# Optimization experiments

Hardware: AMD Instinct MI355X
Metric: run time of the kernel (lower is better)

The kernel has to match this reference:

```python
import jax, jax.numpy as jnp
import numpy as np


def setup_inputs() -> dict:
    key = jax.random.key(0)
    ks = jax.random.split(key, 32)
    B, S, H, E, Vs, T = 32, 400, 512, 300, 200, 32
    EN, V = 50000, 50200
    rn = lambda k, shape, s=0.05: jax.random.normal(k, shape, jnp.float32) * s
    return {
        'encoder_hidden': rn(ks[0], (B, S, 2 * H), 1.0),
        'hidden0': rn(ks[1], (B, H), 1.0),
        'user_embed': rn(ks[2], (B, E), 1.0),
        'W_embed': rn(ks[3], (EN, E), 1.0),
        'W_ih': rn(ks[4], (3 * H, E)), 'W_hh': rn(ks[5], (3 * H, H)),
        'b_ih': rn(ks[6], (3 * H,)), 'b_hh': rn(ks[7], (3 * H,)),
        'Wk_c': rn(ks[8], (2 * H, H)), 'bk_c': rn(ks[9], (H,)),
        'Wq_c': rn(ks[10], (H, H)), 'bq_c': rn(ks[11], (H,)),
        'we_c': rn(ks[12], (H,)), 'be_c': rn(ks[13], (1,)),
        'Wk_u': rn(ks[14], (E, H)), 'bk_u': rn(ks[15], (H,)),
        'Wq_u': rn(ks[16], (H, H)), 'bq_u': rn(ks[17], (H,)),
        'we_u': rn(ks[18], (H,)), 'be_u': rn(ks[19], (1,)),
        'Wc': rn(ks[20], (3 * H + 2 * E, H)),
        'Wg': rn(ks[21], (3 * H + E,)), 'bg': rn(ks[22], (1,)),
        'Wgen': rn(ks[23], (H, EN)),
        'src_mask': jnp.ones((B, S), jnp.int32),
        'tgt_': jax.random.randint(ks[24], (B, T), 0, EN),
        'specific_vocab': jax.random.randint(ks[25], (B, Vs), 0, EN),
        'vocab_size': V,
    }


def reference(encoder_hidden, hidden0, user_embed, W_embed, W_ih, W_hh, b_ih, b_hh,
              Wk_c, bk_c, Wq_c, bq_c, we_c, be_c, Wk_u, bk_u, Wq_u, bq_u, we_u, be_u,
              Wc, Wg, bg, Wgen, src_mask, tgt_, specific_vocab, vocab_size):
    B, T = tgt_.shape
    # teacher forcing: prev token embed, step 0 uses <s> token id 1
    tgt_embed = W_embed[tgt_]                                  # [B,T,E]
    init_embed = jnp.broadcast_to(W_embed[1], (B, 1, W_embed.shape[1]))
    prev = jnp.concatenate([init_embed, tgt_embed[:, :T - 1]], axis=1)
    xs = jnp.swapaxes(prev, 0, 1)                              # [T,B,E]

    user_vocab_emb = W_embed[specific_vocab]                   # [B,Vs,E]
    proj_key_c = encoder_hidden @ Wk_c + bk_c                  # [B,S,H]
    proj_key_u = user_vocab_emb @ Wk_u + bk_u                  # [B,Vs,H]
    mask = src_mask != 0
    batch_idx = jnp.arange(B)[:, None]

    def gru_cell(h, x):
        gi = x @ W_ih.T + b_ih
        gh = h @ W_hh.T + b_hh
        i_r, i_z, i_n = jnp.split(gi, 3, axis=-1)
        h_r, h_z, h_n = jnp.split(gh, 3, axis=-1)
        r = jax.nn.sigmoid(i_r + h_r)
        z = jax.nn.sigmoid(i_z + h_z)
        n = jnp.tanh(i_n + r * h_n)
        return (1.0 - z) * n + z * h

    def step(h, x):
        h = gru_cell(h, x)                                     # [B,H]
        q = h
        # Bahdanau attention over encoder states
        sc = jnp.tanh((q @ Wq_c + bq_c)[:, None, :] + proj_key_c) @ we_c + be_c  # [B,S]
        sc = jnp.where(mask, sc, -1e9)
        ac = jax.nn.softmax(sc, axis=-1)
        ctx_c = jnp.einsum('bs,bsd->bd', ac, encoder_hidden)   # [B,2H]
        # Bahdanau attention over user-specific vocab embeddings
        su = jnp.tanh((q @ Wq_u + bq_u)[:, None, :] + proj_key_u) @ we_u + be_u  # [B,Vs]
        au = jax.nn.softmax(su, axis=-1)
        ctx_u = jnp.einsum('bv,bve->be', au, user_vocab_emb)   # [B,E]
        ch = jnp.tanh(jnp.concatenate([q, ctx_c, ctx_u, user_embed], axis=-1) @ Wc)
        gen_prob = jax.nn.softmax(ch @ Wgen, axis=-1)          # [B,embed_num]
        gen_prob = jnp.pad(gen_prob, ((0, 0), (0, vocab_size - gen_prob.shape[-1])))
        copy_prob = jnp.zeros((B, vocab_size), gen_prob.dtype).at[batch_idx, specific_vocab].add(au)
        copy_p = jax.nn.sigmoid(jnp.concatenate([ctx_c, q, ctx_u], axis=-1) @ Wg + bg[0])[:, None]
        mix = copy_p * copy_prob + (1.0 - copy_p) * gen_prob   # [B,vocab]
        return h, mix

    _, probs = jax.lax.scan(step, hidden0, xs)                 # [T,B,V]
    return jnp.swapaxes(probs, 0, 1)                           # [B,T,V]
```

## Files before the change

kernel.cpp:

```cpp
#include <hip/hip_runtime.h>


typedef __attribute__((ext_vector_type(8))) short short8;
typedef __attribute__((ext_vector_type(4))) float f32x4;
typedef unsigned short us;

__device__ __forceinline__ float bf2f(us u) {
  return __uint_as_float(((unsigned)u) << 16);
}
__device__ __forceinline__ us f2bf(float f) {
  unsigned x = __float_as_uint(f);
  unsigned r = x + 0x7fffu + ((x >> 16) & 1u);
  return (us)(r >> 16);
}
__device__ __forceinline__ float fsigmoid(float x) { return 1.f / (1.f + __expf(-x)); }
__device__ __forceinline__ float ftanh(float x) {
  float t = __expf(-2.f * fabsf(x));
  float r = (1.f - t) / (1.f + t);
  return x >= 0.f ? r : -r;
}
__device__ __forceinline__ float ftanh_fast(float x) {
  float u = __expf(-2.f * fabsf(x));
  float r = (1.f - u) * __builtin_amdgcn_rcpf(1.f + u);
  return copysignf(r, x);
}


__global__ __launch_bounds__(256) void k_cast_f2b(const float* __restrict__ src,
                                                  us* __restrict__ dst, int n4) {
  int stride = gridDim.x * blockDim.x;
  for (int i = blockIdx.x * blockDim.x + threadIdx.x; i < n4; i += stride) {
    float4 v = ((const float4*)src)[i];
    ushort4 o;
    o.x = f2bf(v.x); o.y = f2bf(v.y); o.z = f2bf(v.z); o.w = f2bf(v.w);
    ((ushort4*)dst)[i] = o;
  }
}

__global__ __launch_bounds__(256) void k_tcastX(const float* __restrict__ src0,
                                                us* __restrict__ dst0,
                                                int R, int C, int Rpad,
                                                size_t srcB, size_t dstB) {
  __shared__ float tile[32][33];
  const float* src = src0 + (size_t)blockIdx.z * srcB;
  us* dst = dst0 + (size_t)blockIdx.z * dstB;
  int c0 = blockIdx.x * 32, r0 = blockIdx.y * 32;
  int tx = threadIdx.x & 31, ty = threadIdx.x >> 5;
#pragma unroll
  for (int i = 0; i < 4; ++i) {
    int r = r0 + ty + i * 8, c = c0 + tx;
    tile[ty + i * 8][tx] = (r < R && c < C) ? src[(size_t)r * C + c] : 0.f;
  }
  __syncthreads();
#pragma unroll
  for (int i = 0; i < 4; ++i) {
    int c = c0 + ty + i * 8, rr = r0 + tx;
    if (c < C && rr < Rpad) dst[(size_t)c * Rpad + rr] = f2bf(tile[tx][ty + i * 8]);
  }
}

__global__ __launch_bounds__(256) void k_tcastXb(const us* __restrict__ src0,
                                                 us* __restrict__ dst0,
                                                 int R, int C, int Rpad,
                                                 size_t srcB, size_t dstB) {
  __shared__ us tile[32][33];
  const us* src = src0 + (size_t)blockIdx.z * srcB;
  us* dst = dst0 + (size_t)blockIdx.z * dstB;
  int c0 = blockIdx.x * 32, r0 = blockIdx.y * 32;
  int tx = threadIdx.x & 31, ty = threadIdx.x >> 5;
#pragma unroll
  for (int i = 0; i < 4; ++i) {
    int r = r0 + ty + i * 8, c = c0 + tx;
    tile[ty + i * 8][tx] = (r < R && c < C) ? src[(size_t)r * C + c] : (us)0;
  }
  __syncthreads();
#pragma unroll
  for (int i = 0; i < 4; ++i) {
    int c = c0 + ty + i * 8, rr = r0 + tx;
    if (c < C && rr < Rpad) dst[(size_t)c * Rpad + rr] = tile[tx][ty + i * 8];
  }
}

__global__ __launch_bounds__(64) void k_castpad(const float* __restrict__ src,
                                                us* __restrict__ dst,
                                                int C, int Cpad) {
  int row = blockIdx.x;
  for (int k = threadIdx.x; k < Cpad; k += 64)
    dst[(size_t)row * Cpad + k] = (k < C) ? f2bf(src[(size_t)row * C + k]) : (us)0;
}

__global__ __launch_bounds__(64) void k_gather_xe(const float* __restrict__ W_embed,
                                                  const int* __restrict__ tgt,
                                                  us* __restrict__ xe) {
  int r = blockIdx.x;
  int t = r >> 5, b = r & 31;
  int tok = (t == 0) ? 1 : tgt[b * 32 + (t - 1)];
  const float* src = W_embed + (size_t)tok * 300;
  for (int k = threadIdx.x; k < 320; k += 64)
    xe[(size_t)r * 320 + k] = (k < 300) ? f2bf(src[k]) : (us)0;
}

__global__ __launch_bounds__(64) void k_gather_uve(const float* __restrict__ W_embed,
                                                   const int* __restrict__ sv,
                                                   us* __restrict__ uve) {
  int row = blockIdx.x;
  int tok = sv[row];
  const float* src = W_embed + (size_t)tok * 300;
  for (int k = threadIdx.x; k < 320; k += 64)
    uve[(size_t)row * 320 + k] = (k < 300) ? f2bf(src[k]) : (us)0;
}

__global__ __launch_bounds__(64) void k_fragpack(const float* __restrict__ W,
                                                 us* __restrict__ F) {
  int q = blockIdx.x, lt = blockIdx.y, kt = blockIdx.z, l = threadIdx.x;
  int localrow = lt * 16 + (l & 15);
  int g = localrow >> 6, jj = localrow & 63;
  const float* src = W + (size_t)(g * 512 + q * 64 + jj) * 512 + kt * 32 + (l >> 4) * 8;
  us* dst = F + (((size_t)(q * 12 + lt) * 16 + kt) * 64 + l) * 8;
#pragma unroll
  for (int i = 0; i < 8; ++i) dst[i] = f2bf(src[i]);
}

template <int MODE>
__global__ __launch_bounds__(512) void gemm_bt(const us* __restrict__ A,
                                               const us* __restrict__ BT,
                                               int M, int N, int K, int Ntiles,
                                               const float* __restrict__ bias,
                                               us* __restrict__ outB,
                                               float* __restrict__ outF,
                                               float* __restrict__ rowsum) {
  __shared__ us As[256 * 32];
  __shared__ us Bs[128 * 32];
  __shared__ float rs[256];
  const int tid = threadIdx.x;
  const int lane = tid & 63, wid = tid >> 6;
  const int wr = wid >> 1, wc = wid & 1;
  const int bx = blockIdx.x;
  const int mt = bx / Ntiles, nt = bx - mt * Ntiles;
  const int m0 = mt * 256, n0 = nt * 128;
  f32x4 acc[4][4] = {};
  for (int kk = 0; kk < K; kk += 32) {
    uint4 av0, av1, bv;
    {
      int c = tid, row = c >> 2, c8 = (c & 3) * 8;
      av0 = *(const uint4*)(A + (size_t)(m0 + row) * K + kk + c8);
      c = tid + 512; row = c >> 2; c8 = (c & 3) * 8;
      av1 = *(const uint4*)(A + (size_t)(m0 + row) * K + kk + c8);
      c = tid; row = c >> 2; c8 = (c & 3) * 8;
      int nr = n0 + row; if (nr > N - 1) nr = N - 1;
      bv = *(const uint4*)(BT + (size_t)nr * K + kk + c8);
    }
    __syncthreads();
    ((uint4*)As)[tid] = av0;
    ((uint4*)As)[tid + 512] = av1;
    ((uint4*)Bs)[tid] = bv;
    __syncthreads();
    short8 af[4], bfr[4];
#pragma unroll
    for (int m = 0; m < 4; ++m)
      af[m] = *(const short8*)(As + (wr * 64 + m * 16 + (lane & 15)) * 32 + (lane >> 4) * 8);
#pragma unroll
    for (int n = 0; n < 4; ++n)
      bfr[n] = *(const short8*)(Bs + (wc * 64 + n * 16 + (lane & 15)) * 32 + (lane >> 4) * 8);
#pragma unroll
    for (int m = 0; m < 4; ++m)
#pragma unroll
      for (int n = 0; n < 4; ++n)
        acc[m][n] = __builtin_amdgcn_mfma_f32_16x16x32_bf16(af[m], bfr[n], acc[m][n], 0, 0, 0);
  }
  if (MODE == 0) {
#pragma unroll
    for (int m = 0; m < 4; ++m)
#pragma unroll
      for (int n = 0; n < 4; ++n)
#pragma unroll
        for (int reg = 0; reg < 4; ++reg) {
          int r = m0 + wr * 64 + m * 16 + (lane >> 4) * 4 + reg;
          int c = n0 + wc * 64 + n * 16 + (lane & 15);
          outB[(size_t)r * N + c] = f2bf(acc[m][n][reg] + bias[c]);
        }
  } else {
    if (tid < 256) rs[tid] = 0.f;
    __syncthreads();
#pragma unroll
    for (int m = 0; m < 4; ++m) {
#pragma unroll
      for (int reg = 0; reg < 4; ++reg) {
        int rloc = wr * 64 + m * 16 + (lane >> 4) * 4 + reg;
        int r = m0 + rloc;
        size_t obase = (size_t)((r & 31) * 32 + (r >> 5)) * 50200;
        float s = 0.f;
#pragma unroll
        for (int n = 0; n < 4; ++n) {
          int c = n0 + wc * 64 + n * 16 + (lane & 15);
          if (c < N) {
            float e = __expf(acc[m][n][reg]);
            if (MODE == 1) outF[obase + c] = e;
            else outB[obase + c] = f2bf(e);
            s += e;
          }
        }
        s += __shfl_xor(s, 1, 64); s += __shfl_xor(s, 2, 64);
        s += __shfl_xor(s, 4, 64); s += __shfl_xor(s, 8, 64);
        if ((lane & 15) == 0) atomicAdd(&rs[rloc], s);
      }
    }
    __syncthreads();
    if (tid < 256) atomicAdd(&rowsum[m0 + tid], rs[tid]);
  }
}

template <int MODE>
__global__ __launch_bounds__(256) void gemm_med(const us* __restrict__ A,
                                                const us* __restrict__ BT,
                                                int M, int N, int K, int Ntiles,
                                                const float* __restrict__ bias,
                                                us* __restrict__ outB) {
  __shared__ us As[64 * 32];
  __shared__ us Bs[128 * 32];
  const int tid = threadIdx.x, lane = tid & 63, w = tid >> 6;
  const int bx = blockIdx.x;
  const int mt = bx / Ntiles, nt = bx - mt * Ntiles;
  const int m0 = mt * 64, n0 = nt * 128;
  f32x4 acc[4][2] = {};
  for (int kk = 0; kk < K; kk += 32) {
    uint4 av, bv0, bv1;
    av = *(const uint4*)(A + (size_t)(m0 + (tid >> 2)) * K + kk + (tid & 3) * 8);
    {
      int i0 = tid * 2, i1 = tid * 2 + 1;
      bv0 = *(const uint4*)(BT + (size_t)(n0 + (i0 >> 2)) * K + kk + (i0 & 3) * 8);
      bv1 = *(const uint4*)(BT + (size_t)(n0 + (i1 >> 2)) * K + kk + (i1 & 3) * 8);
    }
    __syncthreads();
    ((uint4*)As)[tid] = av;
    ((uint4*)Bs)[tid * 2] = bv0;
    ((uint4*)Bs)[tid * 2 + 1] = bv1;
    __syncthreads();
    short8 af[4], bf0, bf1;
#pragma unroll
    for (int m = 0; m < 4; ++m)
      af[m] = *(const short8*)(As + (m * 16 + (lane & 15)) * 32 + (lane >> 4) * 8);
    bf0 = *(const short8*)(Bs + ((w * 2 + 0) * 16 + (lane & 15)) * 32 + (lane >> 4) * 8);
    bf1 = *(const short8*)(Bs + ((w * 2 + 1) * 16 + (lane & 15)) * 32 + (lane >> 4) * 8);
#pragma unroll
    for (int m = 0; m < 4; ++m) {
      acc[m][0] = __builtin_amdgcn_mfma_f32_16x16x32_bf16(af[m], bf0, acc[m][0], 0, 0, 0);
      acc[m][1] = __builtin_amdgcn_mfma_f32_16x16x32_bf16(af[m], bf1, acc[m][1], 0, 0, 0);
    }
  }
#pragma unroll
  for (int m = 0; m < 4; ++m)
#pragma unroll
    for (int q = 0; q < 2; ++q)
#pragma unroll
      for (int reg = 0; reg < 4; ++reg) {
        int r = m0 + m * 16 + (lane >> 4) * 4 + reg;
        int c = n0 + (w * 2 + q) * 16 + (lane & 15);
        float v = acc[m][q][reg];
        if (MODE == 0) v += bias[c];
        else v = ftanh_fast(v);
        outB[(size_t)r * N + c] = f2bf(v);
      }
}

struct GP {
  const us* frag; const us* gib; const float* bhh; const float* hidden0;
  us* hball;
  float* hfall;
  int* arrive;
};

__global__ __launch_bounds__(768, 1) void k_gru(GP P) {
  const int q = blockIdx.x;
  const int tid = threadIdx.x;
  const int lane = tid & 63, w = tid >> 6;
  __shared__ us hs[32 * 512];
  __shared__ float gh[192 * 33];
  short8 bfr[16];
  {
    const us* fb = P.frag + (((size_t)(q * 12 + w) * 16) * 64 + lane) * 8;
#pragma unroll
    for (int kt = 0; kt < 16; ++kt) bfr[kt] = *(const short8*)(fb + (size_t)kt * 512);
  }
  float hprev[3];
#pragma unroll
  for (int s = 0; s < 3; ++s) {
    int i = tid + s * 768;
    if (i < 2048) {
      int b = i >> 6, jj = i & 63;
      hprev[s] = P.hidden0[b * 512 + q * 64 + jj];
    }
  }
  const int sw = (lane & 7) << 3;
  for (int t = 0; t < 32; ++t) {
    if (t > 0) {
      if (tid == 0) {
        while (__hip_atomic_load(P.arrive + (t - 1), __ATOMIC_ACQUIRE,
                                 __HIP_MEMORY_SCOPE_AGENT) < 8) {
          __builtin_amdgcn_s_sleep(1);
        }
      }
      __syncthreads();
    }
    const us* hp = P.hball + (size_t)t * 16384;
    for (int i = tid; i < 2048; i += 768)
      ((uint4*)hs)[i ^ ((i >> 6) & 7)] = *(const uint4*)(hp + i * 8);
    __syncthreads();
    f32x4 acc0 = {}, acc1 = {};
#pragma unroll
    for (int kt = 0; kt < 16; ++kt) {
      int base0 = ((lane & 15) * 512 + kt * 32 + (lane >> 4) * 8) ^ sw;
      int base1 = (((lane & 15) + 16) * 512 + kt * 32 + (lane >> 4) * 8) ^ sw;
      short8 a0 = *(const short8*)(hs + base0);
      short8 a1 = *(const short8*)(hs + base1);
      acc0 = __builtin_amdgcn_mfma_f32_16x16x32_bf16(a0, bfr[kt], acc0, 0, 0, 0);
      acc1 = __builtin_amdgcn_mfma_f32_16x16x32_bf16(a1, bfr[kt], acc1, 0, 0, 0);
    }
    {
      int col = w * 16 + (lane & 15);
#pragma unroll
      for (int reg = 0; reg < 4; ++reg) {
        gh[col * 33 + ((lane >> 4) * 4 + reg)] = acc0[reg];
        gh[col * 33 + (16 + (lane >> 4) * 4 + reg)] = acc1[reg];
      }
    }
    __syncthreads();
    us* hbn = P.hball + (size_t)(t + 1) * 16384;
    float* hfn = P.hfall + (size_t)t * 16384;
#pragma unroll
    for (int s = 0; s < 3; ++s) {
      int i = tid + s * 768;
      if (i < 2048) {
        int b = i >> 6, jj = i & 63;
        int j = q * 64 + jj;
        float g0 = gh[jj * 33 + b] + P.bhh[j];
        float g1 = gh[(64 + jj) * 33 + b] + P.bhh[512 + j];
        float g2 = gh[(128 + jj) * 33 + b] + P.bhh[1024 + j];
        size_t gbase = (size_t)(t * 32 + b) * 1536;
        float r_ = fsigmoid(bf2f(P.gib[gbase + j]) + g0);
        float z_ = fsigmoid(bf2f(P.gib[gbase + 512 + j]) + g1);
        float n_ = ftanh(bf2f(P.gib[gbase + 1024 + j]) + r_ * g2);
        float hv = (1.f - z_) * n_ + z_ * hprev[s];
        hprev[s] = hv;
        hbn[b * 512 + j] = f2bf(hv);
        hfn[b * 512 + j] = hv;
      }
    }
    __syncthreads();
    if (tid == 0)
      __hip_atomic_fetch_add(P.arrive + t, 1, __ATOMIC_RELEASE,
                             __HIP_MEMORY_SCOPE_AGENT);
  }
}

__global__ __launch_bounds__(256) void k_scores(const us* __restrict__ Qall,
                                                const us* __restrict__ pkc,
                                                const us* __restrict__ pku,
                                                const float* __restrict__ wec,
                                                const float* __restrict__ bec,
                                                const float* __restrict__ weu,
                                                const float* __restrict__ beu,
                                                const int* __restrict__ src_mask,
                                                float* __restrict__ sc_enc,
                                                float* __restrict__ sc_usr) {
  __shared__ us q[32 * 512];
  const int bid = blockIdx.x;
  const bool enc = bid < 800;
  int b, s0, qoff, S;
  if (enc) { b = bid / 25; s0 = (bid % 25) * 16; qoff = 0; S = 400; }
  else { int j = bid - 800; b = j / 13; s0 = (j % 13) * 16; qoff = 512; S = 200; }
  for (int i = threadIdx.x; i < 2048; i += 256) {
    int tt = i >> 6, c8 = (i & 63) * 8;
    ((uint4*)q)[i] = *(const uint4*)(Qall + (size_t)(tt * 32 + b) * 1024 + qoff + c8);
  }
  const int w = threadIdx.x >> 6, lane = threadIdx.x & 63;
  const int d0 = lane * 8;
  const float* we = enc ? wec : weu;
  float wef[8];
  {
    float4 w0 = *(const float4*)(we + d0);
    float4 w1 = *(const float4*)(we + d0 + 4);
    wef[0] = w0.x; wef[1] = w0.y; wef[2] = w0.z; wef[3] = w0.w;
    wef[4] = w1.x; wef[5] = w1.y; wef[6] = w1.z; wef[7] = w1.w;
  }
  const float bias = enc ? bec[0] : beu[0];
  float pkf[4][8];
  int ss[4], validv[4], maskedv[4];
#pragma unroll
  for (int si = 0; si < 4; ++si) {
    int s = s0 + w * 4 + si;
    validv[si] = (s < S);
    int sc = validv[si] ? s : (S - 1);
    ss[si] = sc;
    const us* pk = enc ? pkc + ((size_t)b * 400 + sc) * 512
                       : pku + ((size_t)b * 200 + sc) * 512;
    uint4 pkv = *(const uint4*)(pk + d0);
    pkf[si][0] = bf2f((us)(pkv.x & 0xffff)); pkf[si][1] = bf2f((us)(pkv.x >> 16));
    pkf[si][2] = bf2f((us)(pkv.y & 0xffff)); pkf[si][3] = bf2f((us)(pkv.y >> 16));
    pkf[si][4] = bf2f((us)(pkv.z & 0xffff)); pkf[si][5] = bf2f((us)(pkv.z >> 16));
    pkf[si][6] = bf2f((us)(pkv.w & 0xffff)); pkf[si][7] = bf2f((us)(pkv.w >> 16));
    maskedv[si] = enc ? (src_mask[b * 400 + sc] == 0) : 0;
  }
  __syncthreads();
  for (int t = 0; t < 32; ++t) {
    short8 qv = *(const short8*)(q + t * 512 + d0);
    float qf[8];
#pragma unroll
    for (int d = 0; d < 8; ++d) qf[d] = bf2f((us)qv[d]);
#pragma unroll
    for (int si = 0; si < 4; ++si) {
      float a = 0.f;
#pragma unroll
      for (int d = 0; d < 8; ++d) {
        float x = qf[d] + pkf[si][d];
        float u = __expf(-2.f * fabsf(x));
        float r2 = (1.f - u) * __builtin_amdgcn_rcpf(1.f + u);
        a = fmaf(copysignf(r2, x), wef[d], a);
      }
#pragma unroll
      for (int m = 1; m < 64; m <<= 1) a += __shfl_xor(a, m, 64);
      if (lane == 0 && validv[si]) {
        float v = a + bias;
        if (enc) sc_enc[(size_t)(t * 32 + b) * 400 + ss[si]] = maskedv[si] ? -1e9f : v;
        else sc_usr[(size_t)(t * 32 + b) * 200 + ss[si]] = v;
      }
    }
  }
}

__device__ __forceinline__ float bmax256(float v, float* r4, int tid) {
#pragma unroll
  for (int m = 1; m < 64; m <<= 1) v = fmaxf(v, __shfl_xor(v, m, 64));
  if ((tid & 63) == 0) r4[tid >> 6] = v;
  __syncthreads();
  float x = fmaxf(fmaxf(r4[0], r4[1]), fmaxf(r4[2], r4[3]));
  __syncthreads();
  return x;
}
__device__ __forceinline__ float bsum256(float v, float* r4, int tid) {
#pragma unroll
  for (int m = 1; m < 64; m <<= 1) v += __shfl_xor(v, m, 64);
  if ((tid & 63) == 0) r4[tid >> 6] = v;
  __syncthreads();
  float x = r4[0] + r4[1] + r4[2] + r4[3];
  __syncthreads();
  return x;
}

__global__ __launch_bounds__(256) void k_softmax(const float* __restrict__ sc_enc,
                                                 const float* __restrict__ sc_usr,
                                                 const float* __restrict__ bg,
                                                 us* __restrict__ AC,
                                                 us* __restrict__ AU,
                                                 float* __restrict__ aual,
                                                 float* __restrict__ cp_acc) {
  __shared__ float r4[4];
  int r = blockIdx.x, tid = threadIdx.x;
  if (r < 1024) {
    int t = r >> 5, b = r & 31;
    float v0 = (tid < 400) ? sc_enc[(size_t)r * 400 + tid] : -3e38f;
    float v1 = (tid + 256 < 400) ? sc_enc[(size_t)r * 400 + tid + 256] : -3e38f;
    float mx = bmax256(fmaxf(v0, v1), r4, tid);
    float e0 = (tid < 400) ? __expf(v0 - mx) : 0.f;
    float e1 = (tid + 256 < 400) ? __expf(v1 - mx) : 0.f;
    float inv = 1.f / bsum256(e0 + e1, r4, tid);
    us* ACb = AC + (size_t)(b * 32 + t) * 416;
    if (tid < 400) ACb[tid] = f2bf(e0 * inv);
    int s2 = tid + 256;
    if (s2 < 400) ACb[s2] = f2bf(e1 * inv);
    else if (s2 < 416) ACb[s2] = 0;
    if (tid == 0) cp_acc[r] = bg[0];
  } else {
    int rr = r - 1024;
    int t = rr >> 5, b = rr & 31;
    float v0 = (tid < 200) ? sc_usr[(size_t)rr * 200 + tid] : -3e38f;
    float mx = bmax256(v0, r4, tid);
    float e0 = (tid < 200) ? __expf(v0 - mx) : 0.f;
    float inv = 1.f / bsum256(e0, r4, tid);
    us* AUb = AU + (size_t)(b * 32 + t) * 224;
    if (tid < 200) {
      float a = e0 * inv;
      AUb[tid] = f2bf(a);
      aual[(size_t)rr * 200 + tid] = a;
    } else if (tid < 224) {
      AUb[tid] = 0;
    }
  }
}

__global__ __launch_bounds__(256) void k_ctx(const us* __restrict__ A,
                                             const us* __restrict__ BT,
                                             const float* __restrict__ Wg,
                                             us* __restrict__ catall,
                                             float* __restrict__ cp_acc,
                                             int N, int Kp, int catOff, int wgOff,
                                             int Nvalid) {
  __shared__ us As[32 * 32];
  __shared__ us Bs[128 * 32];
  __shared__ float gaccs[32];
  const int b = blockIdx.y, n0 = blockIdx.x * 128;
  const us* Ab = A + (size_t)b * 32 * Kp;
  const us* Bb = BT + (size_t)b * N * Kp;
  const int tid = threadIdx.x, lane = tid & 63, w = tid >> 6;
  if (tid < 32) gaccs[tid] = 0.f;
  f32x4 acc[2][2] = {};
  for (int kk = 0; kk < Kp; kk += 32) {
    uint4 av, bv0, bv1;
    if (tid < 128) av = *(const uint4*)(Ab + (size_t)(tid >> 2) * Kp + kk + (tid & 3) * 8);
    {
      int i0 = tid * 2, row0 = i0 >> 2, c0 = (i0 & 3) * 8;
      int i1 = tid * 2 + 1, row1 = i1 >> 2, c1 = (i1 & 3) * 8;
      int nr0 = n0 + row0; if (nr0 > N - 1) nr0 = N - 1;
      int nr1 = n0 + row1; if (nr1 > N - 1) nr1 = N - 1;
      bv0 = *(const uint4*)(Bb + (size_t)nr0 * Kp + kk + c0);
      bv1 = *(const uint4*)(Bb + (size_t)nr1 * Kp + kk + c1);
    }
    __syncthreads();
    if (tid < 128) ((uint4*)As)[tid] = av;
    ((uint4*)Bs)[tid * 2] = bv0;
    ((uint4*)Bs)[tid * 2 + 1] = bv1;
    __syncthreads();
    short8 a0 = *(const short8*)(As + ((lane & 15)) * 32 + (lane >> 4) * 8);
    short8 a1 = *(const short8*)(As + (16 + (lane & 15)) * 32 + (lane >> 4) * 8);
#pragma unroll
    for (int qq = 0; qq < 2; ++qq) {
      short8 bf_ = *(const short8*)(Bs + ((w * 2 + qq) * 16 + (lane & 15)) * 32 + (lane >> 4) * 8);
      acc[0][qq] = __builtin_amdgcn_mfma_f32_16x16x32_bf16(a0, bf_, acc[0][qq], 0, 0, 0);
      acc[1][qq] = __builtin_amdgcn_mfma_f32_16x16x32_bf16(a1, bf_, acc[1][qq], 0, 0, 0);
    }
  }
#pragma unroll
  for (int mt = 0; mt < 2; ++mt)
#pragma unroll
    for (int qq = 0; qq < 2; ++qq)
#pragma unroll
      for (int reg = 0; reg < 4; ++reg) {
        int t_ = mt * 16 + (lane >> 4) * 4 + reg;
        int c = n0 + (w * 2 + qq) * 16 + (lane & 15);
        if (c < Nvalid) {
          float v = acc[mt][qq][reg];
          catall[(size_t)(t_ * 32 + b) * 2144 + catOff + c] = f2bf(v);
          atomicAdd(&gaccs[t_], v * Wg[wgOff + c]);
        }
      }
  __syncthreads();
  if (tid < 32) atomicAdd(&cp_acc[tid * 32 + b], gaccs[tid]);
}

__global__ __launch_bounds__(256) void k_catgate(const us* __restrict__ hball,
                                                 const float* __restrict__ hfall,
                                                 const float* __restrict__ ue,
                                                 const float* __restrict__ Wg,
                                                 const float* __restrict__ cp_acc,
                                                 us* __restrict__ catall,
                                                 float* __restrict__ cp_all) {
  __shared__ float r4[4];
  int r = blockIdx.x, tid = threadIdx.x;
  int t = r >> 5, b = r & 31;
  us* row = catall + (size_t)r * 2144;
  const us* hb = hball + (size_t)(t + 1) * 16384 + b * 512;
  row[tid] = hb[tid];
  row[256 + tid] = hb[256 + tid];
  float gp = 0.f;
  for (int i = tid; i < 512; i += 256)
    gp += hfall[(size_t)t * 16384 + b * 512 + i] * Wg[1024 + i];
  for (int i = tid; i < 308; i += 256)
    row[1836 + i] = (i < 300) ? f2bf(ue[b * 300 + i]) : (us)0;
  float gtot = bsum256(gp, r4, tid);
  if (tid == 0) cp_all[r] = fsigmoid(gtot + cp_acc[r]);
}

__global__ __launch_bounds__(256) void k_finalize(float* __restrict__ out,
                                                  const float* __restrict__ rowsum,
                                                  const float* __restrict__ cp_all,
                                                  const float* __restrict__ au_all,
                                                  const int* __restrict__ sv) {
  int r = blockIdx.x;
  int t = threadIdx.x;
  int b = r & 31, tt = r >> 5;
  float cp = cp_all[r];
  float scale = (1.f - cp) / rowsum[r];
  float* base = out + (size_t)(b * 32 + tt) * 50200;
  float4* b4 = (float4*)base;
  for (int i = t; i < 12550; i += 256) {
    if (i < 12500) {
      float4 v = b4[i];
      v.x *= scale; v.y *= scale; v.z *= scale; v.w *= scale;
      b4[i] = v;
    } else {
      b4[i] = make_float4(0.f, 0.f, 0.f, 0.f);
    }
  }
  __syncthreads();
  if (t < 200) {
    int idx = sv[b * 200 + t];
    atomicAdd(base + idx, cp * au_all[(size_t)r * 200 + t]);
  }
}

__global__ __launch_bounds__(256) void k_finalize2(const us* __restrict__ expb,
                                                   const float* __restrict__ rowsum,
                                                   const float* __restrict__ cp_all,
                                                   const float* __restrict__ au_all,
                                                   const int* __restrict__ sv,
                                                   float* __restrict__ out) {
  int r = blockIdx.x;
  int t = threadIdx.x;
  int b = r & 31, tt = r >> 5;
  float cp = cp_all[r];
  float scale = (1.f - cp) / rowsum[r];
  size_t obase = (size_t)(b * 32 + tt) * 50200;
  const uint4* eb = (const uint4*)(expb + obase);
  float4* ob = (float4*)(out + obase);
  for (int i = t; i < 6275; i += 256) {
    float4 o0, o1;
    if (i < 6250) {
      uint4 ev = eb[i];
      o0.x = bf2f((us)(ev.x & 0xffff)) * scale; o0.y = bf2f((us)(ev.x >> 16)) * scale;
      o0.z = bf2f((us)(ev.y & 0xffff)) * scale; o0.w = bf2f((us)(ev.y >> 16)) * scale;
      o1.x = bf2f((us)(ev.z & 0xffff)) * scale; o1.y = bf2f((us)(ev.z >> 16)) * scale;
      o1.z = bf2f((us)(ev.w & 0xffff)) * scale; o1.w = bf2f((us)(ev.w >> 16)) * scale;
    } else {
      o0 = make_float4(0.f, 0.f, 0.f, 0.f);
      o1 = o0;
    }
    ob[i * 2] = o0;
    ob[i * 2 + 1] = o1;
  }
  __syncthreads();
  if (t < 200) {
    int idx = sv[b * 200 + t];
    atomicAdd(out + obase + idx, cp * au_all[(size_t)r * 200 + t]);
  }
}


extern "C" void kernel_launch(void* const* d_in, const int* in_sizes, int n_in,
                              void* d_out, int out_size, void* d_ws, size_t ws_size,
                              hipStream_t stream) {
  (void)in_sizes; (void)n_in; (void)out_size;
  const float* enc = (const float*)d_in[0];
  const float* hidden0 = (const float*)d_in[1];
  const float* user_embed = (const float*)d_in[2];
  const float* W_embed = (const float*)d_in[3];
  const float* W_ih = (const float*)d_in[4];
  const float* W_hh = (const float*)d_in[5];
  const float* b_ih = (const float*)d_in[6];
  const float* b_hh = (const float*)d_in[7];
  const float* Wk_c = (const float*)d_in[8];
  const float* bk_c = (const float*)d_in[9];
  const float* Wq_c = (const float*)d_in[10];
  const float* bq_c = (const float*)d_in[11];
  const float* we_c = (const float*)d_in[12];
  const float* be_c = (const float*)d_in[13];
  const float* Wk_u = (const float*)d_in[14];
  const float* bk_u = (const float*)d_in[15];
  const float* Wq_u = (const float*)d_in[16];
  const float* bq_u = (const float*)d_in[17];
  const float* we_u = (const float*)d_in[18];
  const float* be_u = (const float*)d_in[19];
  const float* Wc = (const float*)d_in[20];
  const float* Wg = (const float*)d_in[21];
  const float* bg = (const float*)d_in[22];
  const float* Wgen = (const float*)d_in[23];
  const int* src_mask = (const int*)d_in[24];
  const int* tgt = (const int*)d_in[25];
  const int* sv = (const int*)d_in[26];
  float* out = (float*)d_out;

  char* base = (char*)d_ws;
  size_t off = 0;
  auto take = [&](size_t bytes) {
    char* p = base + off;
    off += (bytes + 255) & ~(size_t)255;
    return p;
  };
  us* WT = (us*)take(50000ull * 512 * 2);
  char* R0 = take(32ull * 1024 * 416 * 2);
  us* encb = (us*)R0;
  us* encTp = (us*)R0;
  char* RCD = take(12800ull * 512 * 2 + 6400ull * 512 * 2);
  us* pkc = (us*)RCD;
  us* pku = (us*)(RCD + 12800ull * 512 * 2);
  us* AC = (us*)RCD;
  us* AU = (us*)(RCD + 860160);
  float* aual = (float*)(RCD + 860160 + 458752);
  us* catall = (us*)(RCD + 860160 + 458752 + 819200);
  us* chb = (us*)(RCD + 860160 + 458752 + 819200 + 4390912);
  char* RU = take(6400ull * 320 * 2);
  us* uve = (us*)RU;
  float* sc_enc = (float*)RU;
  float* sc_usr = (float*)(RU + 1024ull * 400 * 4);
  us* uveTp = (us*)take(32ull * 320 * 224 * 2);
  char* RG = take(2700000);
  us* WkcT = (us*)RG;
  us* WihT = (us*)(RG + 1048576);
  us* xe = (us*)(RG + 1048576 + 983040);
  us* Qall = (us*)RG;
  us* WkuT = (us*)take(512ull * 320 * 2);
  us* WqcuT = (us*)take(1024ull * 512 * 2);
  us* WcT = (us*)take(512ull * 2144 * 2);
  us* WhhF = (us*)take(1536ull * 512 * 2);
  us* gib = (us*)take(1024ull * 1536 * 2);
  us* hball = (us*)take(33ull * 16384 * 2);
  float* hfall = (float*)take(32ull * 16384 * 4);
  float* bqcu = (float*)take(1024 * 4);
  float* cp_acc = (float*)take(1024 * 4);
  float* cp_all = (float*)take(1024 * 4);
  float* rsum = (float*)take(1024 * 4);
  int* arrive = (int*)take(32 * 4);
  size_t expb_bytes = 1024ull * 50200 * 2;
  bool use_bf16exp = (ws_size >= off + expb_bytes + 256);
  us* expb = use_bf16exp ? (us*)take(expb_bytes) : nullptr;

  hipMemcpyAsync(bqcu, bq_c, 512 * 4, hipMemcpyDeviceToDevice, stream);
  hipMemcpyAsync(bqcu + 512, bq_u, 512 * 4, hipMemcpyDeviceToDevice, stream);
  hipMemsetAsync(rsum, 0, 1024 * 4, stream);
  hipMemsetAsync(arrive, 0, 32 * 4, stream);

  k_cast_f2b<<<2048, 256, 0, stream>>>(enc, encb, 3276800);
  k_cast_f2b<<<16, 256, 0, stream>>>(hidden0, hball, 4096);
  k_tcastX<<<dim3(1563, 16, 1), 256, 0, stream>>>(Wgen, WT, 512, 50000, 512, 0, 0);
  k_tcastX<<<dim3(16, 32, 1), 256, 0, stream>>>(Wk_c, WkcT, 1024, 512, 1024, 0, 0);
  k_tcastX<<<dim3(16, 10, 1), 256, 0, stream>>>(Wk_u, WkuT, 300, 512, 320, 0, 0);
  k_tcastX<<<dim3(16, 16, 1), 256, 0, stream>>>(Wq_c, WqcuT, 512, 512, 512, 0, 0);
  k_tcastX<<<dim3(16, 16, 1), 256, 0, stream>>>(Wq_u, WqcuT + 512ull * 512, 512, 512, 512, 0, 0);
  k_tcastX<<<dim3(16, 67, 1), 256, 0, stream>>>(Wc, WcT, 2136, 512, 2144, 0, 0);
  k_castpad<<<1536, 64, 0, stream>>>(W_ih, WihT, 300, 320);
  k_fragpack<<<dim3(8, 12, 16), 64, 0, stream>>>(W_hh, WhhF);
  k_gather_xe<<<1024, 64, 0, stream>>>(W_embed, tgt, xe);
  k_gather_uve<<<6400, 64, 0, stream>>>(W_embed, sv, uve);

  gemm_bt<0><<<200, 512, 0, stream>>>(encb, WkcT, 12800, 512, 1024, 4, bk_c, pkc, nullptr, nullptr);
  gemm_bt<0><<<100, 512, 0, stream>>>(uve, WkuT, 6400, 512, 320, 4, bk_u, pku, nullptr, nullptr);
  gemm_med<0><<<192, 256, 0, stream>>>(xe, WihT, 1024, 1536, 320, 12, b_ih, gib);

  k_tcastX<<<dim3(32, 13, 32), 256, 0, stream>>>(enc, encTp, 400, 1024, 416,
                                                 400ull * 1024, 1024ull * 416);
  k_tcastXb<<<dim3(10, 7, 32), 256, 0, stream>>>(uve, uveTp, 200, 320, 224,
                                                 200ull * 320, 320ull * 224);

  GP gp;
  gp.frag = WhhF; gp.gib = gib; gp.bhh = b_hh; gp.hidden0 = hidden0;
  gp.hball = hball; gp.hfall = hfall; gp.arrive = arrive;
  k_gru<<<8, 768, 0, stream>>>(gp);

  gemm_med<0><<<128, 256, 0, stream>>>(hball + 16384, WqcuT, 1024, 1024, 512, 8,
                                       bqcu, Qall);
  k_scores<<<1216, 256, 0, stream>>>(Qall, pkc, pku, we_c, be_c, we_u, be_u,
                                     src_mask, sc_enc, sc_usr);
  k_softmax<<<2048, 256, 0, stream>>>(sc_enc, sc_usr, bg, AC, AU, aual, cp_acc);
  k_ctx<<<dim3(8, 32), 256, 0, stream>>>(AC, encTp, Wg, catall, cp_acc,
                                         1024, 416, 512, 0, 1024);
  k_ctx<<<dim3(3, 32), 256, 0, stream>>>(AU, uveTp, Wg, catall, cp_acc,
                                         320, 224, 1536, 1536, 300);
  k_catgate<<<1024, 256, 0, stream>>>(hball, hfall, user_embed, Wg, cp_acc,
                                      catall, cp_all);
  gemm_med<2><<<64, 256, 0, stream>>>(catall, WcT, 1024, 512, 2144, 4, nullptr, chb);
  if (use_bf16exp) {
    gemm_bt<3><<<4 * 391, 512, 0, stream>>>(chb, WT, 1024, 50000, 512, 391, nullptr,
                                            expb, nullptr, rsum);
    k_finalize2<<<1024, 256, 0, stream>>>(expb, rsum, cp_all, aual, sv, out);
  } else {
    gemm_bt<1><<<4 * 391, 512, 0, stream>>>(chb, WT, 1024, 50000, 512, 391, nullptr,
                                            nullptr, out, rsum);
    k_finalize<<<1024, 256, 0, stream>>>(out, rsum, cp_all, aual, sv);
  }
}
```

Baseline: 787.6 us.

## Fuse GRU recurrence with independent prep kernels into one persistent launch

```diff
diff --git a/kernel.cpp b/kernel.cpp
--- a/kernel.cpp
+++ b/kernel.cpp
@@ -20,7 +20,7 @@
   return x >= 0.f ? r : -r;
 }
 __device__ __forceinline__ float ftanh_fast(float x) {
-  float u = __expf(-2.f * fabsf(x));
+  float u = exp2f(-2.8853900817779268f * fabsf(x));
   float r = (1.f - u) * __builtin_amdgcn_rcpf(1.f + u);
   return copysignf(r, x);
 }
@@ -263,19 +263,20 @@
       }
 }
 
-struct GP {
+struct FP {
   const us* frag; const us* gib; const float* bhh; const float* hidden0;
-  us* hball;
-  float* hfall;
-  int* arrive;
+  us* hball; float* hfall; int* arrive;
+  const us* encb; const us* WkcT; const float* bkc; us* pkc;
+  const us* uve; const us* WkuT; const float* bku; us* pku;
+  const float* Wgen; us* WT;
+  const float* enc; us* encTp;
+  us* uveTp;
 };
 
-__global__ __launch_bounds__(768, 1) void k_gru(GP P) {
-  const int q = blockIdx.x;
-  const int tid = threadIdx.x;
+__device__ void gru_body(const FP& P, int q, int tid, char* pool) {
+  us* hs = (us*)pool;
+  float* gh = (float*)(pool + 32768);
   const int lane = tid & 63, w = tid >> 6;
-  __shared__ us hs[32 * 512];
-  __shared__ float gh[192 * 33];
   short8 bfr[16];
   {
     const us* fb = P.frag + (((size_t)(q * 12 + w) * 16) * 64 + lane) * 8;
@@ -331,8 +332,7 @@
     for (int s = 0; s < 3; ++s) {
       int i = tid + s * 768;
       if (i < 2048) {
-        int b = i >> 6, jj = i & 63;
-        int j = q * 64 + jj;
+        int b = i >> 6, jj = i & 63, j = q * 64 + jj;
         float g0 = gh[jj * 33 + b] + P.bhh[j];
         float g1 = gh[(64 + jj) * 33 + b] + P.bhh[512 + j];
         float g2 = gh[(128 + jj) * 33 + b] + P.bhh[1024 + j];
@@ -350,6 +350,166 @@
     if (tid == 0)
       __hip_atomic_fetch_add(P.arrive + t, 1, __ATOMIC_RELEASE,
                              __HIP_MEMORY_SCOPE_AGENT);
+  }
+}
+
+__device__ void gemm0_body(const us* A, const us* BT, int N, int K,
+                           int mt, int nt, const float* bias, us* outB,
+                           int tid, char* pool) {
+  us* As = (us*)pool;
+  us* Bs = (us*)(pool + 16384);
+  const bool act = tid < 512;
+  const int lane = tid & 63, wid = (tid >> 6) & 7;
+  const int wr = wid >> 1, wc = wid & 1;
+  const int m0 = mt * 256, n0 = nt * 128;
+  f32x4 acc[4][4] = {};
+  for (int kk = 0; kk < K; kk += 32) {
+    uint4 av0 = {0, 0, 0, 0}, av1 = {0, 0, 0, 0}, bv = {0, 0, 0, 0};
+    if (act) {
+      int c = tid, row = c >> 2, c8 = (c & 3) * 8;
+      av0 = *(const uint4*)(A + (size_t)(m0 + row) * K + kk + c8);
+      av1 = *(const uint4*)(A + (size_t)(m0 + 128 + row) * K + kk + c8);
+      int nr = n0 + row; if (nr > N - 1) nr = N - 1;
+      bv = *(const uint4*)(BT + (size_t)nr * K + kk + c8);
+    }
+    __syncthreads();
+    if (act) {
+      ((uint4*)As)[tid] = av0;
+      ((uint4*)As)[tid + 512] = av1;
+      ((uint4*)Bs)[tid] = bv;
+    }
+    __syncthreads();
+    if (act) {
+      short8 af[4], bfr[4];
+#pragma unroll
+      for (int m = 0; m < 4; ++m)
+        af[m] = *(const short8*)(As + (wr * 64 + m * 16 + (lane & 15)) * 32 + (lane >> 4) * 8);
+#pragma unroll
+      for (int n = 0; n < 4; ++n)
+        bfr[n] = *(const short8*)(Bs + (wc * 64 + n * 16 + (lane & 15)) * 32 + (lane >> 4) * 8);
+#pragma unroll
+      for (int m = 0; m < 4; ++m)
+#pragma unroll
+        for (int n = 0; n < 4; ++n)
+          acc[m][n] = __builtin_amdgcn_mfma_f32_16x16x32_bf16(af[m], bfr[n], acc[m][n], 0, 0, 0);
+    }
+  }
+  if (act) {
+#pragma unroll
+    for (int m = 0; m < 4; ++m)
+#pragma unroll
+      for (int n = 0; n < 4; ++n)
+#pragma unroll
+        for (int reg = 0; reg < 4; ++reg) {
+          int r = m0 + wr * 64 + m * 16 + (lane >> 4) * 4 + reg;
+          int c = n0 + wc * 64 + n * 16 + (lane & 15);
+          outB[(size_t)r * N + c] = f2bf(acc[m][n][reg] + bias[c]);
+        }
+  }
+}
+
+__global__ __launch_bounds__(768, 1) void k_fat(FP P) {
+  __shared__ char pool[58368];
+  const int bid = blockIdx.x, tid = threadIdx.x;
+  if (bid < 8) { gru_body(P, bid, tid, pool); return; }
+  if (bid < 208) {
+    int j = bid - 8;
+    gemm0_body(P.encb, P.WkcT, 512, 1024, j >> 2, j & 3, P.bkc, P.pkc, tid, pool);
+    return;
+  }
+  if (bid < 308) {
+    int j = bid - 208;
+    gemm0_body(P.uve, P.WkuT, 512, 320, j >> 2, j & 3, P.bku, P.pku, tid, pool);
+    return;
+  }
+  const int g = tid >> 8, lt = tid & 255;
+  const int tx = lt & 31, ty = lt >> 5;
+  float* tb = (float*)(pool + g * 4224);
+  if (bid < 830) {
+    int base = (bid - 308) * 3 + g;
+    for (int it = 0; it < 16; ++it) {
+      int sub = base + it * 1566;
+      bool valid = sub < 25008;
+      int x = valid ? sub % 1563 : 0, y = valid ? sub / 1563 : 0;
+      int c0 = x * 32, r0 = y * 32;
+      if (valid) {
+#pragma unroll
+        for (int i = 0; i < 4; ++i) {
+          int r = r0 + ty + i * 8, c = c0 + tx;
+          tb[(ty + i * 8) * 33 + tx] =
+              (c < 50000) ? P.Wgen[(size_t)r * 50000 + c] : 0.f;
+        }
+      }
+      __syncthreads();
+      if (valid) {
+#pragma unroll
+        for (int i = 0; i < 4; ++i) {
+          int c = c0 + ty + i * 8;
+          if (c < 50000)
+            P.WT[(size_t)c * 512 + r0 + tx] = f2bf(tb[tx * 33 + ty + i * 8]);
+        }
+      }
+      __syncthreads();
+    }
+    return;
+  }
+  if (bid < 1108) {
+    int base = (bid - 830) * 3 + g;
+    for (int it = 0; it < 16; ++it) {
+      int sub = base + it * 834;
+      bool valid = sub < 13312;
+      int x = sub & 31, rem = sub >> 5;
+      int y = rem % 13, z = rem / 13;
+      const float* src = P.enc + (size_t)z * 409600;
+      us* dst = P.encTp + (size_t)z * 425984;
+      int c0 = x * 32, r0 = y * 32;
+      if (valid) {
+#pragma unroll
+        for (int i = 0; i < 4; ++i) {
+          int r = r0 + ty + i * 8, c = c0 + tx;
+          tb[(ty + i * 8) * 33 + tx] = (r < 400) ? src[(size_t)r * 1024 + c] : 0.f;
+        }
+      }
+      __syncthreads();
+      if (valid) {
+#pragma unroll
+        for (int i = 0; i < 4; ++i) {
+          int c = c0 + ty + i * 8, rr = r0 + tx;
+          if (rr < 416) dst[(size_t)c * 416 + rr] = f2bf(tb[tx * 33 + ty + i * 8]);
+        }
+      }
+      __syncthreads();
+    }
+    return;
+  }
+  {
+    us* tbu = (us*)tb;
+    int base = (bid - 1108) * 3 + g;
+    for (int it = 0; it < 16; ++it) {
+      int sub = base + it * 141;
+      bool valid = sub < 2240;
+      int x = sub % 10, rem = sub / 10;
+      int y = rem % 7, z = rem / 7;
+      const us* src = P.uve + (size_t)z * 64000;
+      us* dst = P.uveTp + (size_t)z * 71680;
+      int c0 = x * 32, r0 = y * 32;
+      if (valid) {
+#pragma unroll
+        for (int i = 0; i < 4; ++i) {
+          int r = r0 + ty + i * 8, c = c0 + tx;
+          tbu[(ty + i * 8) * 33 + tx] = (r < 200) ? src[(size_t)r * 320 + c] : (us)0;
+        }
+      }
+      __syncthreads();
+      if (valid) {
+#pragma unroll
+        for (int i = 0; i < 4; ++i) {
+          int c = c0 + ty + i * 8, rr = r0 + tx;
+          if (rr < 224) dst[(size_t)c * 224 + rr] = tbu[tx * 33 + ty + i * 8];
+        }
+      }
+      __syncthreads();
+    }
   }
 }
 
@@ -413,7 +573,7 @@
 #pragma unroll
       for (int d = 0; d < 8; ++d) {
         float x = qf[d] + pkf[si][d];
-        float u = __expf(-2.f * fabsf(x));
+        float u = exp2f(-2.8853900817779268f * fabsf(x));
         float r2 = (1.f - u) * __builtin_amdgcn_rcpf(1.f + u);
         a = fmaf(copysignf(r2, x), wef[d], a);
       }
@@ -678,7 +838,6 @@
   us* WT = (us*)take(50000ull * 512 * 2);
   char* R0 = take(32ull * 1024 * 416 * 2);
   us* encb = (us*)R0;
-  us* encTp = (us*)R0;
   char* RCD = take(12800ull * 512 * 2 + 6400ull * 512 * 2);
   us* pkc = (us*)RCD;
   us* pku = (us*)(RCD + 12800ull * 512 * 2);
@@ -710,8 +869,9 @@
   float* rsum = (float*)take(1024 * 4);
   int* arrive = (int*)take(32 * 4);
   size_t expb_bytes = 1024ull * 50200 * 2;
-  bool use_bf16exp = (ws_size >= off + expb_bytes + 256);
-  us* expb = use_bf16exp ? (us*)take(expb_bytes) : nullptr;
+  bool big_ws = (ws_size >= off + expb_bytes + 256);
+  us* expb = big_ws ? (us*)take(expb_bytes) : nullptr;
+  us* encTp = big_ws ? expb : (us*)R0;
 
   hipMemcpyAsync(bqcu, bq_c, 512 * 4, hipMemcpyDeviceToDevice, stream);
   hipMemcpyAsync(bqcu + 512, bq_u, 512 * 4, hipMemcpyDeviceToDevice, stream);
@@ -720,7 +880,6 @@
 
   k_cast_f2b<<<2048, 256, 0, stream>>>(enc, encb, 3276800);
   k_cast_f2b<<<16, 256, 0, stream>>>(hidden0, hball, 4096);
-  k_tcastX<<<dim3(1563, 16, 1), 256, 0, stream>>>(Wgen, WT, 512, 50000, 512, 0, 0);
   k_tcastX<<<dim3(16, 32, 1), 256, 0, stream>>>(Wk_c, WkcT, 1024, 512, 1024, 0, 0);
   k_tcastX<<<dim3(16, 10, 1), 256, 0, stream>>>(Wk_u, WkuT, 300, 512, 320, 0, 0);
   k_tcastX<<<dim3(16, 16, 1), 256, 0, stream>>>(Wq_c, WqcuT, 512, 512, 512, 0, 0);
@@ -730,20 +889,29 @@
   k_fragpack<<<dim3(8, 12, 16), 64, 0, stream>>>(W_hh, WhhF);
   k_gather_xe<<<1024, 64, 0, stream>>>(W_embed, tgt, xe);
   k_gather_uve<<<6400, 64, 0, stream>>>(W_embed, sv, uve);
-
-  gemm_bt<0><<<200, 512, 0, stream>>>(encb, WkcT, 12800, 512, 1024, 4, bk_c, pkc, nullptr, nullptr);
-  gemm_bt<0><<<100, 512, 0, stream>>>(uve, WkuT, 6400, 512, 320, 4, bk_u, pku, nullptr, nullptr);
   gemm_med<0><<<192, 256, 0, stream>>>(xe, WihT, 1024, 1536, 320, 12, b_ih, gib);
 
-  k_tcastX<<<dim3(32, 13, 32), 256, 0, stream>>>(enc, encTp, 400, 1024, 416,
-                                                 400ull * 1024, 1024ull * 416);
-  k_tcastXb<<<dim3(10, 7, 32), 256, 0, stream>>>(uve, uveTp, 200, 320, 224,
-                                                 200ull * 320, 320ull * 224);
-
-  GP gp;
-  gp.frag = WhhF; gp.gib = gib; gp.bhh = b_hh; gp.hidden0 = hidden0;
-  gp.hball = hball; gp.hfall = hfall; gp.arrive = arrive;
-  k_gru<<<8, 768, 0, stream>>>(gp);
+  FP fp;
+  fp.frag = WhhF; fp.gib = gib; fp.bhh = b_hh; fp.hidden0 = hidden0;
+  fp.hball = hball; fp.hfall = hfall; fp.arrive = arrive;
+  fp.encb = encb; fp.WkcT = WkcT; fp.bkc = bk_c; fp.pkc = pkc;
+  fp.uve = uve; fp.WkuT = WkuT; fp.bku = bk_u; fp.pku = pku;
+  fp.Wgen = Wgen; fp.WT = WT; fp.enc = enc; fp.encTp = encTp; fp.uveTp = uveTp;
+
+  if (big_ws) {
+    k_fat<<<1155, 768, 0, stream>>>(fp);
+  } else {
+    k_tcastX<<<dim3(1563, 16, 1), 256, 0, stream>>>(Wgen, WT, 512, 50000, 512, 0, 0);
+    gemm_bt<0><<<200, 512, 0, stream>>>(encb, WkcT, 12800, 512, 1024, 4, bk_c, pkc,
+                                        nullptr, nullptr);
+    gemm_bt<0><<<100, 512, 0, stream>>>(uve, WkuT, 6400, 512, 320, 4, bk_u, pku,
+                                        nullptr, nullptr);
+    k_tcastX<<<dim3(32, 13, 32), 256, 0, stream>>>(enc, encTp, 400, 1024, 416,
+                                                   400ull * 1024, 1024ull * 416);
+    k_tcastXb<<<dim3(10, 7, 32), 256, 0, stream>>>(uve, uveTp, 200, 320, 224,
+                                                   200ull * 320, 320ull * 224);
+    k_fat<<<8, 768, 0, stream>>>(fp);
+  }
 
   gemm_med<0><<<128, 256, 0, stream>>>(hball + 16384, WqcuT, 1024, 1024, 512, 8,
                                        bqcu, Qall);
@@ -757,7 +925,7 @@
   k_catgate<<<1024, 256, 0, stream>>>(hball, hfall, user_embed, Wg, cp_acc,
                                       catall, cp_all);
   gemm_med<2><<<64, 256, 0, stream>>>(catall, WcT, 1024, 512, 2144, 4, nullptr, chb);
-  if (use_bf16exp) {
+  if (big_ws) {
     gemm_bt<3><<<4 * 391, 512, 0, stream>>>(chb, WT, 1024, 50000, 512, 391, nullptr,
                                             expb, nullptr, rsum);
     k_finalize2<<<1024, 256, 0, stream>>>(expb, rsum, cp_all, aual, sv, out);
```

Measured after the change: 735.2 us. 6.7% less time.
